# Kernel tuning notes

Measured on AMD Instinct MI355X. Metric: run time of the kernel, lower is better.

## Reference

```python
import jax, jax.numpy as jnp
import numpy as np

N = 100000
E = 640000
D = 128      # node_dim == edge_dim
H = 256      # conv MLP hidden dim
EPS = 1e-5


def _ln(x, g, b):
    mu = jnp.mean(x, axis=-1, keepdims=True)
    var = jnp.var(x, axis=-1, keepdims=True)
    return (x - mu) * jax.lax.rsqrt(var + EPS) * g + b


def _conv_mlp(x, W1, b1, g1, be1, W2, b2, g2, be2):
    h = _ln(x @ W1 + b1, g1, be1)          # (N, H)
    h = jax.nn.relu(h)
    return _ln(h @ W2 + b2, g2, be2)        # (N, D)


def setup_inputs() -> dict:
    key = jax.random.key(0)
    ks = jax.random.split(key, 6)
    s1 = 1.0 / np.sqrt(D)
    s2 = 1.0 / np.sqrt(H)
    return {
        "x": jax.random.normal(ks[0], (N, D), dtype=jnp.float32),
        "edge_index": jax.random.randint(ks[1], (2, E), 0, N, dtype=jnp.int32),
        "edge_attr": jax.random.normal(ks[2], (E, D), dtype=jnp.float32),
        "W1": jax.random.uniform(ks[3], (D, H), jnp.float32, -s1, s1),
        "b1": jnp.zeros((H,), jnp.float32),
        "g1": jnp.ones((H,), jnp.float32),
        "be1": jnp.zeros((H,), jnp.float32),
        "W2": jax.random.uniform(ks[4], (H, D), jnp.float32, -s2, s2),
        "b2": jnp.zeros((D,), jnp.float32),
        "g2": jnp.ones((D,), jnp.float32),
        "be2": jnp.zeros((D,), jnp.float32),
        "g_out": jnp.ones((D,), jnp.float32),
        "b_out": jnp.zeros((D,), jnp.float32),
    }


def reference(x, edge_index, edge_attr, W1, b1, g1, be1, W2, b2, g2, be2, g_out, b_out):
    # Conv(h[w]) for all nodes once, then gather per edge (vectorized form of
    # the per-node/per-neighbor loops in the torch module).
    conv = _conv_mlp(x, W1, b1, g1, be1, W2, b2, g2, be2)   # (N, D)
    src, dst = edge_index[0], edge_index[1]
    msgs = conv[dst] * edge_attr                            # (E, D): Conv(h[w]) * e[v,w]
    agg = jax.ops.segment_sum(msgs, src, num_segments=N)    # scatter-add into v
    return _ln(agg + x, g_out, b_out)
```

## Files before the change

### kernel.cpp

```cpp
#include <hip/hip_runtime.h>

constexpr int D = 128;
constexpr int H = 256;
constexpr float EPS = 1e-5f;

typedef __attribute__((ext_vector_type(8))) __bf16  bf16x8;
typedef __attribute__((ext_vector_type(4))) float   f32x4;

static __device__ __forceinline__ unsigned short f2bfu(float f) {
    unsigned u = __float_as_uint(f);
    return (unsigned short)((u + 0x7FFFu + ((u >> 16) & 1u)) >> 16);
}
static __device__ __forceinline__ float bf2f(unsigned short u) {
    return __uint_as_float((unsigned)u << 16);
}

static __device__ __forceinline__ f32x4 mfma16x16x32(bf16x8 a, bf16x8 b, f32x4 c) {
    return __builtin_amdgcn_mfma_f32_16x16x32_bf16(a, b, c, 0, 0, 0);
}

static __device__ __forceinline__ void pack_w_elem(
    const float* __restrict__ W, unsigned short* __restrict__ Wp, int K, int Ncols, int e)
{
    int i  = e & 7;
    int l  = (e >> 3) & 63;
    int jt = e >> 9;
    int nt = K >> 5;
    int j  = jt / nt;
    int t  = jt - j * nt;
    int k  = 32 * t + ((l >> 4) << 3) + i;
    int c  = 16 * j + (l & 15);
    Wp[e] = f2bfu(W[(size_t)k * Ncols + c]);
}

__global__ __launch_bounds__(256) void prep_kernel(
    const float* __restrict__ W1, unsigned short* __restrict__ W1p,
    const float* __restrict__ W2, unsigned short* __restrict__ W2p,
    int* __restrict__ counts, int* __restrict__ cnt0, int N, int zeroBlocks)
{
    int b = blockIdx.x;
    if (b < 128) {
        pack_w_elem(W1, W1p, D, H, b * 256 + threadIdx.x);
    } else if (b < 256) {
        pack_w_elem(W2, W2p, H, D, (b - 128) * 256 + threadIdx.x);
    } else if (b < 256 + zeroBlocks) {
        int i = (b - 256) * 256 + threadIdx.x;
        if (i < N) counts[i] = 0;
    } else {
        int i = (b - 256 - zeroBlocks) * 256 + threadIdx.x;
        if (i < N) cnt0[i] = 0;
    }
}

__global__ __launch_bounds__(256) void conv_hist_kernel(
    const float* __restrict__ x,
    const unsigned short* __restrict__ W1p, const float* __restrict__ b1,
    const float* __restrict__ g1, const float* __restrict__ be1,
    const unsigned short* __restrict__ W2p, const float* __restrict__ b2,
    const float* __restrict__ g2, const float* __restrict__ be2,
    unsigned short* __restrict__ convb, int N,
    const int* __restrict__ eidx, int* __restrict__ counts, int E, int convBlocks)
{
    __shared__ unsigned short Hs[64 * 256];
    __shared__ unsigned short Ws[2][8192];

    if ((int)blockIdx.x >= convBlocks) {
        int e = (blockIdx.x - convBlocks) * 256 + threadIdx.x;
        if (e < E) atomicAdd(&counts[eidx[e]], 1);
        return;
    }

    const int wv   = threadIdx.x >> 6;
    const int lane = threadIdx.x & 63;
    const int rrow = lane & 15;
    const int kgrp = lane >> 4;
    const int r0   = blockIdx.x * 64 + wv * 16;

    float4 sv0, sv1, sv2, sv3;
    auto issueW = [&](const unsigned short* Wp, int c) {
        const float4* s = (const float4*)(Wp + c * 8192);
        sv0 = s[threadIdx.x];
        sv1 = s[threadIdx.x + 256];
        sv2 = s[threadIdx.x + 512];
        sv3 = s[threadIdx.x + 768];
    };
    auto writeS = [&](int b) {
        float4* d = (float4*)Ws[b];
        d[threadIdx.x]       = sv0;
        d[threadIdx.x + 256] = sv1;
        d[threadIdx.x + 512] = sv2;
        d[threadIdx.x + 768] = sv3;
    };

    int arow = r0 + rrow; if (arow >= N) arow = N - 1;
    const float* xr = x + (size_t)arow * D + kgrp * 8;
    bf16x8 A1[4];
    #pragma unroll
    for (int t = 0; t < 4; ++t) {
        float4 fa = *(const float4*)(xr + t * 32);
        float4 fb = *(const float4*)(xr + t * 32 + 4);
        bf16x8 a;
        a[0] = (__bf16)fa.x; a[1] = (__bf16)fa.y; a[2] = (__bf16)fa.z; a[3] = (__bf16)fa.w;
        a[4] = (__bf16)fb.x; a[5] = (__bf16)fb.y; a[6] = (__bf16)fb.z; a[7] = (__bf16)fb.w;
        A1[t] = a;
    }

    f32x4 acc[16];
    #pragma unroll
    for (int j = 0; j < 16; ++j) acc[j] = (f32x4){0.f, 0.f, 0.f, 0.f};

    issueW(W1p, 0); writeS(0); __syncthreads();
    #pragma unroll
    for (int c = 0; c < 4; ++c) {
        if (c < 3) issueW(W1p, c + 1);
        #pragma unroll
        for (int jj = 0; jj < 4; ++jj) {
            #pragma unroll
            for (int t = 0; t < 4; ++t) {
                bf16x8 B = *(const bf16x8*)((const char*)Ws[c & 1]
                             + ((jj * 4 + t) * 512 + lane * 8) * 2);
                acc[c * 4 + jj] = mfma16x16x32(A1[t], B, acc[c * 4 + jj]);
            }
        }
        if (c < 3) writeS((c + 1) & 1);
        __syncthreads();
    }

    float b1r[16], g1r[16], be1r[16];
    #pragma unroll
    for (int j = 0; j < 16; ++j) {
        int c = 16 * j + rrow;
        b1r[j] = b1[c]; g1r[j] = g1[c]; be1r[j] = be1[c];
    }

    float s1[4] = {0,0,0,0}, s2[4] = {0,0,0,0};
    #pragma unroll
    for (int j = 0; j < 16; ++j) {
        #pragma unroll
        for (int r = 0; r < 4; ++r) {
            float v = acc[j][r] + b1r[j];
            acc[j][r] = v;
            s1[r] += v; s2[r] += v * v;
        }
    }
    #pragma unroll
    for (int m = 1; m < 16; m <<= 1) {
        #pragma unroll
        for (int r = 0; r < 4; ++r) {
            s1[r] += __shfl_xor(s1[r], m);
            s2[r] += __shfl_xor(s2[r], m);
        }
    }

    issueW(W2p, 0);

    #pragma unroll
    for (int r = 0; r < 4; ++r) {
        float mu  = s1[r] * (1.f / H);
        float var = s2[r] * (1.f / H) - mu * mu;
        float rs  = rsqrtf(var + EPS);
        int row = wv * 16 + kgrp * 4 + r;
        #pragma unroll
        for (int j = 0; j < 16; ++j) {
            float h = fmaxf((acc[j][r] - mu) * rs * g1r[j] + be1r[j], 0.f);
            int byte = (row << 9) + ((16 * j + rrow) << 1);
            byte ^= (row & 15) << 4;
            *(unsigned short*)((char*)Hs + byte) = f2bfu(h);
        }
    }

    bf16x8 A2[8];
    #pragma unroll
    for (int t = 0; t < 8; ++t) {
        int row  = wv * 16 + rrow;
        int byte = (row << 9) + ((t * 32 + kgrp * 8) << 1);
        byte ^= (row & 15) << 4;
        A2[t] = *(const bf16x8*)((const char*)Hs + byte);
    }

    writeS(0); __syncthreads();

    f32x4 acc2[8];
    #pragma unroll
    for (int j = 0; j < 8; ++j) acc2[j] = (f32x4){0.f, 0.f, 0.f, 0.f};
    #pragma unroll
    for (int c = 0; c < 4; ++c) {
        if (c < 3) issueW(W2p, c + 1);
        #pragma unroll
        for (int jj = 0; jj < 2; ++jj) {
            #pragma unroll
            for (int t = 0; t < 8; ++t) {
                bf16x8 B = *(const bf16x8*)((const char*)Ws[c & 1]
                             + ((jj * 8 + t) * 512 + lane * 8) * 2);
                acc2[c * 2 + jj] = mfma16x16x32(A2[t], B, acc2[c * 2 + jj]);
            }
        }
        if (c < 3) writeS((c + 1) & 1);
        __syncthreads();
    }

    float b2r[8], g2r[8], be2r[8];
    #pragma unroll
    for (int j = 0; j < 8; ++j) {
        int c = 16 * j + rrow;
        b2r[j] = b2[c]; g2r[j] = g2[c]; be2r[j] = be2[c];
    }

    float u1[4] = {0,0,0,0}, u2[4] = {0,0,0,0};
    #pragma unroll
    for (int j = 0; j < 8; ++j) {
        #pragma unroll
        for (int r = 0; r < 4; ++r) {
            float v = acc2[j][r] + b2r[j];
            acc2[j][r] = v;
            u1[r] += v; u2[r] += v * v;
        }
    }
    #pragma unroll
    for (int m = 1; m < 16; m <<= 1) {
        #pragma unroll
        for (int r = 0; r < 4; ++r) {
            u1[r] += __shfl_xor(u1[r], m);
            u2[r] += __shfl_xor(u2[r], m);
        }
    }

    #pragma unroll
    for (int r = 0; r < 4; ++r) {
        float mu  = u1[r] * (1.f / D);
        float var = u2[r] * (1.f / D) - mu * mu;
        float rs  = rsqrtf(var + EPS);
        int row = wv * 16 + kgrp * 4 + r;
        #pragma unroll
        for (int j = 0; j < 8; ++j) {
            float o = (acc2[j][r] - mu) * rs * g2r[j] + be2r[j];
            int byte = (row << 9) + ((16 * j + rrow) << 1);
            byte ^= (row & 15) << 4;
            *(unsigned short*)((char*)Hs + byte) = f2bfu(o);
        }
    }

    {
        int lrow = wv * 16 + (lane >> 2);
        int grow = r0 + (lane >> 2);
        if (grow < N) {
            #pragma unroll
            for (int k = 0; k < 4; ++k) {
                int chunk = k * 4 + (lane & 3);
                int byte  = (lrow << 9) + (chunk << 4);
                byte ^= (lrow & 15) << 4;
                uint4 v = *(const uint4*)((const char*)Hs + byte);
                *(uint4*)(convb + (size_t)grow * D + chunk * 8) = v;
            }
        }
    }
}

__global__ __launch_bounds__(256) void scan1_kernel(
    const int* __restrict__ counts, int* __restrict__ row_part,
    int* __restrict__ bsums, int N)
{
    __shared__ int sd[256];
    int t  = threadIdx.x;
    int i0 = blockIdx.x * 1024 + t * 4;
    int c0 = (i0+0 < N) ? counts[i0+0] : 0;
    int c1 = (i0+1 < N) ? counts[i0+1] : 0;
    int c2 = (i0+2 < N) ? counts[i0+2] : 0;
    int c3 = (i0+3 < N) ? counts[i0+3] : 0;
    int s  = c0 + c1 + c2 + c3;
    sd[t] = s;
    __syncthreads();
    #pragma unroll
    for (int off = 1; off < 256; off <<= 1) {
        int v = (t >= off) ? sd[t - off] : 0;
        __syncthreads();
        sd[t] += v;
        __syncthreads();
    }
    int ex = sd[t] - s;
    if (i0+0 < N) row_part[i0+0] = ex;
    if (i0+1 < N) row_part[i0+1] = ex + c0;
    if (i0+2 < N) row_part[i0+2] = ex + c0 + c1;
    if (i0+3 < N) row_part[i0+3] = ex + c0 + c1 + c2;
    if (t == 255) bsums[blockIdx.x] = sd[255];
}

__global__ __launch_bounds__(128) void scan2_kernel(int* __restrict__ bsums, int NB)
{
    __shared__ int sd[128];
    int t = threadIdx.x;
    int v = (t < NB) ? bsums[t] : 0;
    sd[t] = v;
    __syncthreads();
    #pragma unroll
    for (int off = 1; off < 128; off <<= 1) {
        int u = (t >= off) ? sd[t - off] : 0;
        __syncthreads();
        sd[t] += u;
        __syncthreads();
    }
    if (t < NB) bsums[t] = sd[t] - v;
}

__global__ __launch_bounds__(256) void fill_kernel(
    const int* __restrict__ eidx,
    const int* __restrict__ row_part, const int* __restrict__ bsums,
    int* __restrict__ cnt0, int2* __restrict__ edat, int E)
{
    int e = blockIdx.x * blockDim.x + threadIdx.x;
    if (e < E) {
        int s    = eidx[e];
        int base = row_part[s] + bsums[s >> 10];
        int p    = base + atomicAdd(&cnt0[s], 1);
        edat[p]  = make_int2(e, eidx[E + e]);
    }
}

__global__ __launch_bounds__(256) void gather_ln_kernel(
    const float* __restrict__ x, const unsigned short* __restrict__ convb,
    const float* __restrict__ eattr,
    const int* __restrict__ row_part, const int* __restrict__ bsums,
    const int2* __restrict__ edat,
    const float* __restrict__ g, const float* __restrict__ b,
    float* __restrict__ out, int N, int E, int totalWaves)
{
    int waveId = blockIdx.x * 4 + (threadIdx.x >> 6);
    int lane = threadIdx.x & 63;
    int half = lane >> 5;
    int c4   = (lane & 31) * 4;

    float4 gv = *(const float4*)(g + c4);
    float4 bv = *(const float4*)(b + c4);

    for (int node = waveId; node < N; node += totalWaves) {
        int jb = row_part[node] + bsums[node >> 10];
        int je = (node + 1 < N) ? (row_part[node + 1] + bsums[(node + 1) >> 10]) : E;

        float4 xv = make_float4(0.f, 0.f, 0.f, 0.f);
        if (half == 0) xv = *(const float4*)(x + (size_t)node * D + c4);

        float4 acc = make_float4(0.f, 0.f, 0.f, 0.f);
        int j = jb + half;

        for (; j + 2 < je; j += 4) {
            int2 ea = edat[j];
            int2 eb = edat[j + 2];
            ushort4 ca = *(const ushort4*)(convb + (size_t)ea.y * D + c4);
            float4  aa = *(const float4*) (eattr + (size_t)ea.x * D + c4);
            ushort4 cb = *(const ushort4*)(convb + (size_t)eb.y * D + c4);
            float4  ab = *(const float4*) (eattr + (size_t)eb.x * D + c4);
            acc.x += bf2f(ca.x) * aa.x; acc.y += bf2f(ca.y) * aa.y;
            acc.z += bf2f(ca.z) * aa.z; acc.w += bf2f(ca.w) * aa.w;
            acc.x += bf2f(cb.x) * ab.x; acc.y += bf2f(cb.y) * ab.y;
            acc.z += bf2f(cb.z) * ab.z; acc.w += bf2f(cb.w) * ab.w;
        }
        if (j < je) {
            int2 ea = edat[j];
            ushort4 ca = *(const ushort4*)(convb + (size_t)ea.y * D + c4);
            float4  aa = *(const float4*) (eattr + (size_t)ea.x * D + c4);
            acc.x += bf2f(ca.x) * aa.x; acc.y += bf2f(ca.y) * aa.y;
            acc.z += bf2f(ca.z) * aa.z; acc.w += bf2f(ca.w) * aa.w;
        }

        acc.x += xv.x; acc.y += xv.y; acc.z += xv.z; acc.w += xv.w;

        acc.x += __shfl_xor(acc.x, 32);
        acc.y += __shfl_xor(acc.y, 32);
        acc.z += __shfl_xor(acc.z, 32);
        acc.w += __shfl_xor(acc.w, 32);

        float s1 = acc.x + acc.y + acc.z + acc.w;
        float s2 = acc.x*acc.x + acc.y*acc.y + acc.z*acc.z + acc.w*acc.w;
        #pragma unroll
        for (int o = 1; o < 32; o <<= 1) {
            s1 += __shfl_xor(s1, o);
            s2 += __shfl_xor(s2, o);
        }
        float mu  = s1 * (1.f / D);
        float var = s2 * (1.f / D) - mu * mu;
        float rs  = rsqrtf(var + EPS);
        if (half == 0) {
            float4 o4;
            o4.x = (acc.x - mu) * rs * gv.x + bv.x;
            o4.y = (acc.y - mu) * rs * gv.y + bv.y;
            o4.z = (acc.z - mu) * rs * gv.z + bv.z;
            o4.w = (acc.w - mu) * rs * gv.w + bv.w;
            *(float4*)(out + (size_t)node * D + c4) = o4;
        }
    }
}

extern "C" void kernel_launch(void* const* d_in, const int* in_sizes, int n_in,
                              void* d_out, int out_size, void* d_ws, size_t ws_size,
                              hipStream_t stream) {
    const float* x     = (const float*)d_in[0];
    const int*   eidx  = (const int*)  d_in[1];
    const float* eattr = (const float*)d_in[2];
    const float* W1    = (const float*)d_in[3];
    const float* b1    = (const float*)d_in[4];
    const float* g1    = (const float*)d_in[5];
    const float* be1   = (const float*)d_in[6];
    const float* W2    = (const float*)d_in[7];
    const float* b2    = (const float*)d_in[8];
    const float* g2    = (const float*)d_in[9];
    const float* be2   = (const float*)d_in[10];
    const float* g_out = (const float*)d_in[11];
    const float* b_out = (const float*)d_in[12];

    const int N = in_sizes[0] / D;
    const int E = in_sizes[1] / 2;

    float* out = (float*)d_out;

    auto align_up = [](size_t v) { return (v + 255) & ~(size_t)255; };
    size_t convB = align_up((size_t)N * D * sizeof(unsigned short));
    size_t cntB  = align_up((size_t)N * sizeof(int));
    size_t rsB   = align_up((size_t)N * sizeof(int));
    size_t c0B   = align_up((size_t)N * sizeof(int));
    size_t bsB   = align_up(128 * sizeof(int));
    size_t edB   = align_up((size_t)E * sizeof(int2));
    size_t w1B   = align_up((size_t)D * H * sizeof(unsigned short));

    char* w = (char*)d_ws;
    unsigned short* convb    = (unsigned short*)(w);
    int*            counts   = (int*)(w + convB);
    int*            row_part = (int*)(w + convB + cntB);
    int*            cnt0     = (int*)(w + convB + cntB + rsB);
    int*            bsums    = (int*)(w + convB + cntB + rsB + c0B);
    int2*           edat     = (int2*)(w + convB + cntB + rsB + c0B + bsB);
    unsigned short* W1p      = (unsigned short*)(w + convB + cntB + rsB + c0B + bsB + edB);
    unsigned short* W2p      = (unsigned short*)(w + convB + cntB + rsB + c0B + bsB + edB + w1B);

    int zeroBlocks = (N + 255) / 256;
    prep_kernel<<<256 + 2 * zeroBlocks, 256, 0, stream>>>(
        W1, W1p, W2, W2p, counts, cnt0, N, zeroBlocks);

    int convBlocks = (N + 63) / 64;
    int histBlocks = (E + 255) / 256;
    conv_hist_kernel<<<convBlocks + histBlocks, 256, 0, stream>>>(
        x, W1p, b1, g1, be1, W2p, b2, g2, be2, convb, N, eidx, counts, E, convBlocks);

    int NB = (N + 1023) / 1024;
    scan1_kernel<<<NB, 256, 0, stream>>>(counts, row_part, bsums, N);
    scan2_kernel<<<1, 128, 0, stream>>>(bsums, NB);

    fill_kernel<<<(E + 255) / 256, 256, 0, stream>>>(
        eidx, row_part, bsums, cnt0, edat, E);

    int gBlocks = 2048;
    int totalWaves = gBlocks * 4;
    gather_ln_kernel<<<gBlocks, 256, 0, stream>>>(
        x, convb, eattr, row_part, bsums, edat, g_out, b_out, out, N, E, totalWaves);
}
```

Measured before the change: 208.1 us.

## Make conv MLP kernel persistent with both weight matrices resident in LDS

Turns the fused conv and histogram kernel into a persistent kernel with 256 blocks. Each block copies all of packed W1 and W2 into 160KB of dynamic shared memory once, then loops over 64-row tiles, prefetching the next tile's x rows while it runs the second GEMM. Edge histogram atomics run in a grid-stride loop after the tiles instead of in separate blocks. This removes the per-block streaming of the weights and the double-buffer barriers. In exchange, occupancy drops to one 4-wave block per CU, so memory latency is harder to hide. The single copy loop also assumes W2p sits directly after W1p in the workspace.

```diff
diff --git a/kernel.cpp b/kernel.cpp
--- a/kernel.cpp
+++ b/kernel.cpp
@@ -59,72 +59,26 @@
     const unsigned short* __restrict__ W2p, const float* __restrict__ b2,
     const float* __restrict__ g2, const float* __restrict__ be2,
     unsigned short* __restrict__ convb, int N,
-    const int* __restrict__ eidx, int* __restrict__ counts, int E, int convBlocks)
-{
-    __shared__ unsigned short Hs[64 * 256];
-    __shared__ unsigned short Ws[2][8192];
-
-    if ((int)blockIdx.x >= convBlocks) {
-        int e = (blockIdx.x - convBlocks) * 256 + threadIdx.x;
-        if (e < E) atomicAdd(&counts[eidx[e]], 1);
-        return;
-    }
+    const int* __restrict__ eidx, int* __restrict__ counts, int E, int nTiles)
+{
+    extern __shared__ unsigned short Sh[];
+    unsigned short* W1s = Sh;
+    unsigned short* W2s = Sh + 32768;
+    unsigned short* Hs  = Sh + 65536;
+
+    {
+        const float4* src = (const float4*)W1p;
+        float4*       dst = (float4*)Sh;
+        #pragma unroll
+        for (int i = 0; i < 32; ++i)
+            dst[threadIdx.x + 256 * i] = src[threadIdx.x + 256 * i];
+    }
+    __syncthreads();
 
     const int wv   = threadIdx.x >> 6;
     const int lane = threadIdx.x & 63;
     const int rrow = lane & 15;
     const int kgrp = lane >> 4;
-    const int r0   = blockIdx.x * 64 + wv * 16;
-
-    float4 sv0, sv1, sv2, sv3;
-    auto issueW = [&](const unsigned short* Wp, int c) {
-        const float4* s = (const float4*)(Wp + c * 8192);
-        sv0 = s[threadIdx.x];
-        sv1 = s[threadIdx.x + 256];
-        sv2 = s[threadIdx.x + 512];
-        sv3 = s[threadIdx.x + 768];
-    };
-    auto writeS = [&](int b) {
-        float4* d = (float4*)Ws[b];
-        d[threadIdx.x]       = sv0;
-        d[threadIdx.x + 256] = sv1;
-        d[threadIdx.x + 512] = sv2;
-        d[threadIdx.x + 768] = sv3;
-    };
-
-    int arow = r0 + rrow; if (arow >= N) arow = N - 1;
-    const float* xr = x + (size_t)arow * D + kgrp * 8;
-    bf16x8 A1[4];
-    #pragma unroll
-    for (int t = 0; t < 4; ++t) {
-        float4 fa = *(const float4*)(xr + t * 32);
-        float4 fb = *(const float4*)(xr + t * 32 + 4);
-        bf16x8 a;
-        a[0] = (__bf16)fa.x; a[1] = (__bf16)fa.y; a[2] = (__bf16)fa.z; a[3] = (__bf16)fa.w;
-        a[4] = (__bf16)fb.x; a[5] = (__bf16)fb.y; a[6] = (__bf16)fb.z; a[7] = (__bf16)fb.w;
-        A1[t] = a;
-    }
-
-    f32x4 acc[16];
-    #pragma unroll
-    for (int j = 0; j < 16; ++j) acc[j] = (f32x4){0.f, 0.f, 0.f, 0.f};
-
-    issueW(W1p, 0); writeS(0); __syncthreads();
-    #pragma unroll
-    for (int c = 0; c < 4; ++c) {
-        if (c < 3) issueW(W1p, c + 1);
-        #pragma unroll
-        for (int jj = 0; jj < 4; ++jj) {
-            #pragma unroll
-            for (int t = 0; t < 4; ++t) {
-                bf16x8 B = *(const bf16x8*)((const char*)Ws[c & 1]
-                             + ((jj * 4 + t) * 512 + lane * 8) * 2);
-                acc[c * 4 + jj] = mfma16x16x32(A1[t], B, acc[c * 4 + jj]);
-            }
-        }
-        if (c < 3) writeS((c + 1) & 1);
-        __syncthreads();
-    }
 
     float b1r[16], g1r[16], be1r[16];
     #pragma unroll
@@ -132,73 +86,6 @@
         int c = 16 * j + rrow;
         b1r[j] = b1[c]; g1r[j] = g1[c]; be1r[j] = be1[c];
     }
-
-    float s1[4] = {0,0,0,0}, s2[4] = {0,0,0,0};
-    #pragma unroll
-    for (int j = 0; j < 16; ++j) {
-        #pragma unroll
-        for (int r = 0; r < 4; ++r) {
-            float v = acc[j][r] + b1r[j];
-            acc[j][r] = v;
-            s1[r] += v; s2[r] += v * v;
-        }
-    }
-    #pragma unroll
-    for (int m = 1; m < 16; m <<= 1) {
-        #pragma unroll
-        for (int r = 0; r < 4; ++r) {
-            s1[r] += __shfl_xor(s1[r], m);
-            s2[r] += __shfl_xor(s2[r], m);
-        }
-    }
-
-    issueW(W2p, 0);
-
-    #pragma unroll
-    for (int r = 0; r < 4; ++r) {
-        float mu  = s1[r] * (1.f / H);
-        float var = s2[r] * (1.f / H) - mu * mu;
-        float rs  = rsqrtf(var + EPS);
-        int row = wv * 16 + kgrp * 4 + r;
-        #pragma unroll
-        for (int j = 0; j < 16; ++j) {
-            float h = fmaxf((acc[j][r] - mu) * rs * g1r[j] + be1r[j], 0.f);
-            int byte = (row << 9) + ((16 * j + rrow) << 1);
-            byte ^= (row & 15) << 4;
-            *(unsigned short*)((char*)Hs + byte) = f2bfu(h);
-        }
-    }
-
-    bf16x8 A2[8];
-    #pragma unroll
-    for (int t = 0; t < 8; ++t) {
-        int row  = wv * 16 + rrow;
-        int byte = (row << 9) + ((t * 32 + kgrp * 8) << 1);
-        byte ^= (row & 15) << 4;
-        A2[t] = *(const bf16x8*)((const char*)Hs + byte);
-    }
-
-    writeS(0); __syncthreads();
-
-    f32x4 acc2[8];
-    #pragma unroll
-    for (int j = 0; j < 8; ++j) acc2[j] = (f32x4){0.f, 0.f, 0.f, 0.f};
-    #pragma unroll
-    for (int c = 0; c < 4; ++c) {
-        if (c < 3) issueW(W2p, c + 1);
-        #pragma unroll
-        for (int jj = 0; jj < 2; ++jj) {
-            #pragma unroll
-            for (int t = 0; t < 8; ++t) {
-                bf16x8 B = *(const bf16x8*)((const char*)Ws[c & 1]
-                             + ((jj * 8 + t) * 512 + lane * 8) * 2);
-                acc2[c * 2 + jj] = mfma16x16x32(A2[t], B, acc2[c * 2 + jj]);
-            }
-        }
-        if (c < 3) writeS((c + 1) & 1);
-        __syncthreads();
-    }
-
     float b2r[8], g2r[8], be2r[8];
     #pragma unroll
     for (int j = 0; j < 8; ++j) {
@@ -206,54 +93,154 @@
         b2r[j] = b2[c]; g2r[j] = g2[c]; be2r[j] = be2[c];
     }
 
-    float u1[4] = {0,0,0,0}, u2[4] = {0,0,0,0};
-    #pragma unroll
-    for (int j = 0; j < 8; ++j) {
+    auto loadA1 = [&](int t0, bf16x8 A[4]) {
+        int arow = t0 * 64 + wv * 16 + rrow; if (arow >= N) arow = N - 1;
+        const float* xr = x + (size_t)arow * D + kgrp * 8;
+        #pragma unroll
+        for (int t = 0; t < 4; ++t) {
+            float4 fa = *(const float4*)(xr + t * 32);
+            float4 fb = *(const float4*)(xr + t * 32 + 4);
+            bf16x8 a;
+            a[0] = (__bf16)fa.x; a[1] = (__bf16)fa.y; a[2] = (__bf16)fa.z; a[3] = (__bf16)fa.w;
+            a[4] = (__bf16)fb.x; a[5] = (__bf16)fb.y; a[6] = (__bf16)fb.z; a[7] = (__bf16)fb.w;
+            A[t] = a;
+        }
+    };
+
+    bf16x8 A1[4], A1n[4];
+    int tile = blockIdx.x;
+    if (tile < nTiles) loadA1(tile, A1);
+
+    while (tile < nTiles) {
+        const int r0 = tile * 64 + wv * 16;
+
+        f32x4 acc[16];
+        #pragma unroll
+        for (int j = 0; j < 16; ++j) acc[j] = (f32x4){0.f, 0.f, 0.f, 0.f};
+        #pragma unroll
+        for (int j = 0; j < 16; ++j) {
+            #pragma unroll
+            for (int t = 0; t < 4; ++t) {
+                bf16x8 B = *(const bf16x8*)((const char*)W1s
+                             + ((j * 4 + t) * 512 + lane * 8) * 2);
+                acc[j] = mfma16x16x32(A1[t], B, acc[j]);
+            }
+        }
+
+        float s1[4] = {0,0,0,0}, s2[4] = {0,0,0,0};
+        #pragma unroll
+        for (int j = 0; j < 16; ++j) {
+            #pragma unroll
+            for (int r = 0; r < 4; ++r) {
+                float v = acc[j][r] + b1r[j];
+                acc[j][r] = v;
+                s1[r] += v; s2[r] += v * v;
+            }
+        }
+        #pragma unroll
+        for (int m = 1; m < 16; m <<= 1) {
+            #pragma unroll
+            for (int r = 0; r < 4; ++r) {
+                s1[r] += __shfl_xor(s1[r], m);
+                s2[r] += __shfl_xor(s2[r], m);
+            }
+        }
+
         #pragma unroll
         for (int r = 0; r < 4; ++r) {
-            float v = acc2[j][r] + b2r[j];
-            acc2[j][r] = v;
-            u1[r] += v; u2[r] += v * v;
-        }
-    }
-    #pragma unroll
-    for (int m = 1; m < 16; m <<= 1) {
+            float mu  = s1[r] * (1.f / H);
+            float var = s2[r] * (1.f / H) - mu * mu;
+            float rs  = rsqrtf(var + EPS);
+            int row = wv * 16 + kgrp * 4 + r;
+            #pragma unroll
+            for (int j = 0; j < 16; ++j) {
+                float h = fmaxf((acc[j][r] - mu) * rs * g1r[j] + be1r[j], 0.f);
+                int byte = (row << 9) + ((16 * j + rrow) << 1);
+                byte ^= (row & 15) << 4;
+                *(unsigned short*)((char*)Hs + byte) = f2bfu(h);
+            }
+        }
+
+        bf16x8 A2[8];
+        #pragma unroll
+        for (int t = 0; t < 8; ++t) {
+            int row  = wv * 16 + rrow;
+            int byte = (row << 9) + ((t * 32 + kgrp * 8) << 1);
+            byte ^= (row & 15) << 4;
+            A2[t] = *(const bf16x8*)((const char*)Hs + byte);
+        }
+
+        int nextTile = tile + (int)gridDim.x;
+        if (nextTile < nTiles) loadA1(nextTile, A1n);
+
+        f32x4 acc2[8];
+        #pragma unroll
+        for (int j = 0; j < 8; ++j) acc2[j] = (f32x4){0.f, 0.f, 0.f, 0.f};
+        #pragma unroll
+        for (int j = 0; j < 8; ++j) {
+            #pragma unroll
+            for (int t = 0; t < 8; ++t) {
+                bf16x8 B = *(const bf16x8*)((const char*)W2s
+                             + ((j * 8 + t) * 512 + lane * 8) * 2);
+                acc2[j] = mfma16x16x32(A2[t], B, acc2[j]);
+            }
+        }
+
+        float u1[4] = {0,0,0,0}, u2[4] = {0,0,0,0};
+        #pragma unroll
+        for (int j = 0; j < 8; ++j) {
+            #pragma unroll
+            for (int r = 0; r < 4; ++r) {
+                float v = acc2[j][r] + b2r[j];
+                acc2[j][r] = v;
+                u1[r] += v; u2[r] += v * v;
+            }
+        }
+        #pragma unroll
+        for (int m = 1; m < 16; m <<= 1) {
+            #pragma unroll
+            for (int r = 0; r < 4; ++r) {
+                u1[r] += __shfl_xor(u1[r], m);
+                u2[r] += __shfl_xor(u2[r], m);
+            }
+        }
         #pragma unroll
         for (int r = 0; r < 4; ++r) {
-            u1[r] += __shfl_xor(u1[r], m);
-            u2[r] += __shfl_xor(u2[r], m);
-        }
-    }
-
-    #pragma unroll
-    for (int r = 0; r < 4; ++r) {
-        float mu  = u1[r] * (1.f / D);
-        float var = u2[r] * (1.f / D) - mu * mu;
-        float rs  = rsqrtf(var + EPS);
-        int row = wv * 16 + kgrp * 4 + r;
-        #pragma unroll
-        for (int j = 0; j < 8; ++j) {
-            float o = (acc2[j][r] - mu) * rs * g2r[j] + be2r[j];
-            int byte = (row << 9) + ((16 * j + rrow) << 1);
-            byte ^= (row & 15) << 4;
-            *(unsigned short*)((char*)Hs + byte) = f2bfu(o);
-        }
-    }
-
-    {
-        int lrow = wv * 16 + (lane >> 2);
-        int grow = r0 + (lane >> 2);
-        if (grow < N) {
-            #pragma unroll
-            for (int k = 0; k < 4; ++k) {
-                int chunk = k * 4 + (lane & 3);
-                int byte  = (lrow << 9) + (chunk << 4);
-                byte ^= (lrow & 15) << 4;
-                uint4 v = *(const uint4*)((const char*)Hs + byte);
-                *(uint4*)(convb + (size_t)grow * D + chunk * 8) = v;
-            }
-        }
-    }
+            float mu  = u1[r] * (1.f / D);
+            float var = u2[r] * (1.f / D) - mu * mu;
+            float rs  = rsqrtf(var + EPS);
+            int row = wv * 16 + kgrp * 4 + r;
+            #pragma unroll
+            for (int j = 0; j < 8; ++j) {
+                float o = (acc2[j][r] - mu) * rs * g2r[j] + be2r[j];
+                int byte = (row << 9) + ((16 * j + rrow) << 1);
+                byte ^= (row & 15) << 4;
+                *(unsigned short*)((char*)Hs + byte) = f2bfu(o);
+            }
+        }
+
+        {
+            int lrow = wv * 16 + (lane >> 2);
+            int grow = r0 + (lane >> 2);
+            if (grow < N) {
+                #pragma unroll
+                for (int k = 0; k < 4; ++k) {
+                    int chunk = k * 4 + (lane & 3);
+                    int byte  = (lrow << 9) + (chunk << 4);
+                    byte ^= (lrow & 15) << 4;
+                    uint4 v = *(const uint4*)((const char*)Hs + byte);
+                    *(uint4*)(convb + (size_t)grow * D + chunk * 8) = v;
+                }
+            }
+        }
+
+        #pragma unroll
+        for (int t = 0; t < 4; ++t) A1[t] = A1n[t];
+        tile = nextTile;
+    }
+
+    for (int e = blockIdx.x * 256 + threadIdx.x; e < E; e += (int)gridDim.x * 256)
+        atomicAdd(&counts[eidx[e]], 1);
 }
 
 __global__ __launch_bounds__(256) void scan1_kernel(
@@ -435,10 +422,12 @@
     prep_kernel<<<256 + 2 * zeroBlocks, 256, 0, stream>>>(
         W1, W1p, W2, W2p, counts, cnt0, N, zeroBlocks);
 
-    int convBlocks = (N + 63) / 64;
-    int histBlocks = (E + 255) / 256;
-    conv_hist_kernel<<<convBlocks + histBlocks, 256, 0, stream>>>(
-        x, W1p, b1, g1, be1, W2p, b2, g2, be2, convb, N, eidx, counts, E, convBlocks);
+    int nTiles = (N + 63) / 64;
+    size_t shBytes = 160 * 1024;
+    hipFuncSetAttribute((const void*)conv_hist_kernel,
+                        hipFuncAttributeMaxDynamicSharedMemorySize, (int)shBytes);
+    conv_hist_kernel<<<256, 256, shBytes, stream>>>(
+        x, W1p, b1, g1, be1, W2p, b2, g2, be2, convb, N, eidx, counts, E, nTiles);
 
     int NB = (N + 1023) / 1024;
     scan1_kernel<<<NB, 256, 0, stream>>>(counts, row_part, bsums, N);
```

Result: slower. 218.0 us (+4.8%).
